# Performance work log

Measured on AMD Instinct MI355X. Metric: run time of the kernel, lower is better.

Reference implementation:

```python
import jax, jax.numpy as jnp
import numpy as np

N = 4096           # batch size (square similarity matrix)
NUM_BINS = 10      # histogram bins (module default)
NUM_CLASSES = 64   # classes used to synthesize the relevance matrix


def setup_inputs() -> dict:
    key = jax.random.key(0)
    k1, k2 = jax.random.split(key)
    # cosine similarities in [-1, 1]
    batch = jax.random.uniform(k1, (N, N), jnp.float32, -1.0, 1.0)
    # relevance matrix from class labels: labels[i,j] = 1 if same class
    cls = jax.random.randint(k2, (N,), 0, NUM_CLASSES)
    labels = (cls[:, None] == cls[None, :]).astype(jnp.float32)
    return {"batch": batch, "labels": labels}


def reference(batch, labels):
    num_bins = NUM_BINS
    I_pos = labels
    I_neg = 1.0 - labels
    N_pos = jnp.sum(labels, axis=1)                      # [N]
    dist2 = 2.0 - 2.0 * jnp.clip(batch, -1.0, 1.0)       # [N, N], in [0, 4]
    Delta = 4.0 / num_bins
    Z = jnp.linspace(0.0, 4.0, num_bins + 1)             # [L], L = num_bins+1

    # soft binning pulse for all bins at once: [N, N, L]
    pulse = jnp.maximum(0.0, 1.0 - jnp.abs(dist2[..., None] - Z) / Delta)
    h_pos = jnp.einsum('nml,nm->nl', pulse, I_pos)       # [N, L]
    h_neg = jnp.einsum('nml,nm->nl', pulse, I_neg)       # [N, L]

    H_pos = jnp.cumsum(h_pos, axis=1)
    H = jnp.cumsum(h_pos + h_neg, axis=1)

    # FastAP = h_pos * H_pos / H, with nan/inf (H == 0) set to 0
    safe_H = jnp.where(H > 0, H, 1.0)
    ap_terms = jnp.where(H > 0, h_pos * H_pos / safe_H, 0.0)

    safe_Np = jnp.where(N_pos > 0, N_pos, 1.0)
    ap = jnp.sum(ap_terms, axis=1) / safe_Np             # [N]

    # drop NaN rows (N_pos == 0) from the mean, matching FastAP[~isnan]
    valid = N_pos > 0
    mean_ap = jnp.sum(jnp.where(valid, ap, 0.0)) / jnp.sum(valid.astype(ap.dtype))
    return 1.0 - mean_ap
```

## Files before the change

kernel.cpp:

```cpp
#include <hip/hip_runtime.h>

#define N 4096
#define NBINS 10
#define BLOCK 256
#define NSLOTS 64
#define GROUPS 4
#define GF4 4

__global__ __launch_bounds__(BLOCK) void fastap_cid_kernel(
    const float* __restrict__ labels, unsigned short* __restrict__ cid,
    float* __restrict__ slots)
{
    if (blockIdx.x == 0 && threadIdx.x < NSLOTS)
        slots[threadIdx.x * 16] = 0.f;

    const int lane = threadIdx.x & 63;
    const int wid  = (blockIdx.x * BLOCK + threadIdx.x) >> 6;
    #pragma unroll
    for (int rr = 0; rr < 4; ++rr) {
        const int row = wid * 4 + rr;
        const float4* l4 = (const float4*)(labels + (size_t)row * N);
        bool done = false;
        for (int r = 0; !done; ++r) {
            float4 v = l4[r * 64 + lane];
            bool any = (v.x > 0.5f) || (v.y > 0.5f) || (v.z > 0.5f) || (v.w > 0.5f);
            unsigned long long m = __ballot(any);
            if (m) {
                int fl = __builtin_ctzll(m);
                if (lane == fl) {
                    int e = (v.x > 0.5f) ? 0 : (v.y > 0.5f) ? 1 : (v.z > 0.5f) ? 2 : 3;
                    cid[row] = (unsigned short)(r * 256 + lane * 4 + e);
                }
                done = true;
            }
        }
    }
}

__global__ __launch_bounds__(BLOCK) void fastap_row_kernel(
    const float* __restrict__ batch, const unsigned short* __restrict__ cid,
    float* __restrict__ slots)
{
    const int tid  = threadIdx.x;
    const int lane = tid & 63;
    const int row  = (blockIdx.x * BLOCK + tid) >> 6;

    const float4*  b4 = (const float4*)(batch + (size_t)row * N);
    const ushort4* c4 = (const ushort4*)cid;
    const int myc = (int)cid[row];

    ushort4 cv[16];
    #pragma unroll
    for (int j = 0; j < 16; ++j) cv[j] = c4[j * 64 + lane];

    float4 buf[2][GF4];
    #pragma unroll
    for (int i = 0; i < GF4; ++i) buf[0][i] = b4[i * 64 + lane];

    unsigned mlo = 0u, mhi = 0u;
    #pragma unroll
    for (int j = 0; j < 8; ++j) {
        mlo |= ((int)cv[j].x == myc ? 1u : 0u) << (j * 4 + 0);
        mlo |= ((int)cv[j].y == myc ? 1u : 0u) << (j * 4 + 1);
        mlo |= ((int)cv[j].z == myc ? 1u : 0u) << (j * 4 + 2);
        mlo |= ((int)cv[j].w == myc ? 1u : 0u) << (j * 4 + 3);
    }
    #pragma unroll
    for (int j = 8; j < 16; ++j) {
        mhi |= ((int)cv[j].x == myc ? 1u : 0u) << ((j - 8) * 4 + 0);
        mhi |= ((int)cv[j].y == myc ? 1u : 0u) << ((j - 8) * 4 + 1);
        mhi |= ((int)cv[j].z == myc ? 1u : 0u) << ((j - 8) * 4 + 2);
        mhi |= ((int)cv[j].w == myc ? 1u : 0u) << ((j - 8) * 4 + 3);
    }

    float hc_pos[NBINS], hc_all[NBINS];
    #pragma unroll
    for (int l = 0; l < NBINS; ++l) { hc_pos[l] = 0.f; hc_all[l] = 0.f; }

    #pragma unroll
    for (int g = 0; g < GROUPS; ++g) {
        if (g + 1 < GROUPS) {
            #pragma unroll
            for (int i = 0; i < GF4; ++i)
                buf[(g + 1) & 1][i] = b4[((g + 1) * GF4 + i) * 64 + lane];
        }
        const unsigned mw = (g < 2) ? mlo : mhi;
        #pragma unroll
        for (int i = 0; i < GF4; ++i) {
            #pragma unroll
            for (int e = 0; e < 4; ++e) {
                float x   = ((const float*)&buf[g & 1][i])[e];
                float lbl = (float)((mw >> ((g & 1) * 16 + i * 4 + e)) & 1u);
                float u = fmaf(5.f, x, -4.f);
                #pragma unroll
                for (int l = 0; l < NBINS; ++l) {
                    float c = fminf(fmaxf(u + (float)l, 0.f), 1.f);
                    hc_pos[l] = fmaf(c, lbl, hc_pos[l]);
                    hc_all[l] += c;
                }
            }
        }
    }

    float np = (float)(__popc(mlo) + __popc(mhi));

    #pragma unroll
    for (int off = 1; off < 64; off <<= 1) {
        #pragma unroll
        for (int l = 0; l < NBINS; ++l) {
            hc_pos[l] += __shfl_xor(hc_pos[l], off, 64);
            hc_all[l] += __shfl_xor(hc_all[l], off, 64);
        }
        np += __shfl_xor(np, off, 64);
    }

    if (lane == 0) {
        float Hp_prev = 0.f, ap = 0.f;
        #pragma unroll
        for (int l = 0; l < NBINS; ++l) {
            float Hp = hc_pos[l];
            float Ha = hc_all[l];
            float hp = Hp - Hp_prev;
            if (Ha > 0.f) ap += hp * Hp / Ha;
            Hp_prev = Hp;
        }
        float Np = np;
        ap += (Np - Hp_prev) * Np * (1.f / (float)N);
        atomicAdd(&slots[(row & (NSLOTS - 1)) * 16], ap / Np);
    }
}

__global__ void fastap_finalize(const float* __restrict__ slots,
                                float* __restrict__ out)
{
    const int lane = threadIdx.x;
    float v = slots[lane * 16];
    #pragma unroll
    for (int off = 32; off > 0; off >>= 1)
        v += __shfl_down(v, off, 64);
    if (lane == 0) out[0] = 1.f - v * (1.f / (float)N);
}

extern "C" void kernel_launch(void* const* d_in, const int* in_sizes, int n_in,
                              void* d_out, int out_size, void* d_ws, size_t ws_size,
                              hipStream_t stream) {
    const float* batch  = (const float*)d_in[0];
    const float* labels = (const float*)d_in[1];
    unsigned short* cid = (unsigned short*)d_ws;
    float* slots = (float*)((char*)d_ws + 8192);
    fastap_cid_kernel<<<N / (4 * 4), BLOCK, 0, stream>>>(labels, cid, slots);
    fastap_row_kernel<<<N / 4, BLOCK, 0, stream>>>(batch, cid, slots);
    fastap_finalize<<<1, 64, 0, stream>>>(slots, (float*)d_out);
}
```

Baseline: 141.4 us.

## Pack histogram math into float2 vectors and fuse finalize via last-block counter

```diff
diff --git a/kernel.cpp b/kernel.cpp
--- a/kernel.cpp
+++ b/kernel.cpp
@@ -7,12 +7,20 @@
 #define GROUPS 4
 #define GF4 4
 
+typedef float f32x2 __attribute__((ext_vector_type(2)));
+
+
 __global__ __launch_bounds__(BLOCK) void fastap_cid_kernel(
     const float* __restrict__ labels, unsigned short* __restrict__ cid,
-    float* __restrict__ slots)
+    float* __restrict__ slots, unsigned* __restrict__ slot_cnt,
+    unsigned* __restrict__ gcnt)
 {
-    if (blockIdx.x == 0 && threadIdx.x < NSLOTS)
-        slots[threadIdx.x * 16] = 0.f;
+    if (blockIdx.x == 0) {
+        if (threadIdx.x < NSLOTS) slots[threadIdx.x * 16] = 0.f;
+        if (threadIdx.x >= 64 && threadIdx.x < 64 + NSLOTS)
+            slot_cnt[threadIdx.x - 64] = 0u;
+        if (threadIdx.x == 128) *gcnt = 0u;
+    }
 
     const int lane = threadIdx.x & 63;
     const int wid  = (blockIdx.x * BLOCK + threadIdx.x) >> 6;
@@ -39,7 +47,8 @@
 
 __global__ __launch_bounds__(BLOCK) void fastap_row_kernel(
     const float* __restrict__ batch, const unsigned short* __restrict__ cid,
-    float* __restrict__ slots)
+    float* __restrict__ slots, unsigned* __restrict__ slot_cnt,
+    unsigned* __restrict__ gcnt, float* __restrict__ out)
 {
     const int tid  = threadIdx.x;
     const int lane = tid & 63;
@@ -73,9 +82,12 @@
         mhi |= ((int)cv[j].w == myc ? 1u : 0u) << ((j - 8) * 4 + 3);
     }
 
-    float hc_pos[NBINS], hc_all[NBINS];
+    f32x2 hp2[NBINS], ha2[NBINS];
     #pragma unroll
-    for (int l = 0; l < NBINS; ++l) { hc_pos[l] = 0.f; hc_all[l] = 0.f; }
+    for (int l = 0; l < NBINS; ++l) {
+        hp2[l] = (f32x2)(0.f);
+        ha2[l] = (f32x2)(0.f);
+    }
 
     #pragma unroll
     for (int g = 0; g < GROUPS; ++g) {
@@ -87,16 +99,25 @@
         const unsigned mw = (g < 2) ? mlo : mhi;
         #pragma unroll
         for (int i = 0; i < GF4; ++i) {
+            const float4 v = buf[g & 1][i];
             #pragma unroll
-            for (int e = 0; e < 4; ++e) {
-                float x   = ((const float*)&buf[g & 1][i])[e];
-                float lbl = (float)((mw >> ((g & 1) * 16 + i * 4 + e)) & 1u);
-                float u = fmaf(5.f, x, -4.f);
+            for (int h = 0; h < 2; ++h) {
+                f32x2 x2;
+                x2.x = (h == 0) ? v.x : v.z;
+                x2.y = (h == 0) ? v.y : v.w;
+                const unsigned bsh = (unsigned)((g & 1) * 16 + i * 4 + h * 2);
+                f32x2 lbl2;
+                lbl2.x = (float)((mw >> bsh) & 1u);
+                lbl2.y = (float)((mw >> (bsh + 1)) & 1u);
+                f32x2 u2 = x2 * 5.f - 4.f;
                 #pragma unroll
                 for (int l = 0; l < NBINS; ++l) {
-                    float c = fminf(fmaxf(u + (float)l, 0.f), 1.f);
-                    hc_pos[l] = fmaf(c, lbl, hc_pos[l]);
-                    hc_all[l] += c;
+                    f32x2 t = u2 + (float)l;
+                    f32x2 c;
+                    c.x = fminf(fmaxf(t.x, 0.f), 1.f);
+                    c.y = fminf(fmaxf(t.y, 0.f), 1.f);
+                    hp2[l] += c * lbl2;
+                    ha2[l] += c;
                 }
             }
         }
@@ -104,6 +125,12 @@
 
     float np = (float)(__popc(mlo) + __popc(mhi));
 
+    float hc_pos[NBINS], hc_all[NBINS];
+    #pragma unroll
+    for (int l = 0; l < NBINS; ++l) {
+        hc_pos[l] = hp2[l].x + hp2[l].y;
+        hc_all[l] = ha2[l].x + ha2[l].y;
+    }
     #pragma unroll
     for (int off = 1; off < 64; off <<= 1) {
         #pragma unroll
@@ -114,6 +141,7 @@
         np += __shfl_xor(np, off, 64);
     }
 
+    int lastflag = 0;
     if (lane == 0) {
         float Hp_prev = 0.f, ap = 0.f;
         #pragma unroll
@@ -126,19 +154,26 @@
         }
         float Np = np;
         ap += (Np - Hp_prev) * Np * (1.f / (float)N);
-        atomicAdd(&slots[(row & (NSLOTS - 1)) * 16], ap / Np);
+
+        const int s = row & (NSLOTS - 1);
+        atomicAdd(&slots[s * 16], ap / Np);
+        __threadfence();
+        unsigned c = atomicAdd(&slot_cnt[s], 1u);
+        if (c == (N / NSLOTS) - 1) {
+            __threadfence();
+            unsigned g = atomicAdd(gcnt, 1u);
+            lastflag = (g == NSLOTS - 1) ? 1 : 0;
+        }
     }
-}
-
-__global__ void fastap_finalize(const float* __restrict__ slots,
-                                float* __restrict__ out)
-{
-    const int lane = threadIdx.x;
-    float v = slots[lane * 16];
-    #pragma unroll
-    for (int off = 32; off > 0; off >>= 1)
-        v += __shfl_down(v, off, 64);
-    if (lane == 0) out[0] = 1.f - v * (1.f / (float)N);
+    lastflag = __shfl(lastflag, 0, 64);
+    if (lastflag) {
+        __threadfence();
+        float v = slots[lane * 16];
+        #pragma unroll
+        for (int off = 32; off > 0; off >>= 1)
+            v += __shfl_down(v, off, 64);
+        if (lane == 0) out[0] = 1.f - v * (1.f / (float)N);
+    }
 }
 
 extern "C" void kernel_launch(void* const* d_in, const int* in_sizes, int n_in,
@@ -147,8 +182,10 @@
     const float* batch  = (const float*)d_in[0];
     const float* labels = (const float*)d_in[1];
     unsigned short* cid = (unsigned short*)d_ws;
-    float* slots = (float*)((char*)d_ws + 8192);
-    fastap_cid_kernel<<<N / (4 * 4), BLOCK, 0, stream>>>(labels, cid, slots);
-    fastap_row_kernel<<<N / 4, BLOCK, 0, stream>>>(batch, cid, slots);
-    fastap_finalize<<<1, 64, 0, stream>>>(slots, (float*)d_out);
+    float* slots    = (float*)((char*)d_ws + 8192);
+    unsigned* scnt  = (unsigned*)((char*)d_ws + 12288);
+    unsigned* gcnt  = (unsigned*)((char*)d_ws + 12544);
+    fastap_cid_kernel<<<N / (4 * 4), BLOCK, 0, stream>>>(labels, cid, slots, scnt, gcnt);
+    fastap_row_kernel<<<N / 4, BLOCK, 0, stream>>>(batch, cid, slots, scnt, gcnt,
+                                                   (float*)d_out);
 }
```

Measured after the change: 267.6 us. +89.2%, slower.
